# Kernel optimization log

Hardware: AMD Instinct MI355X
Metric: run time of the kernel (lower is better)

Reference implementation:

```python
import jax, jax.numpy as jnp
import numpy as np

B, T, DZ = 128, 512, 512  # batch, timesteps, latent state dim


def setup_inputs() -> dict:
    key = jax.random.key(0)
    k1, k2, k3 = jax.random.split(key, 3)
    t_inputs = jax.random.normal(k1, (B, T, 1), dtype=jnp.float32)      # per-step scalar time signal
    init_states = jax.random.normal(k2, (B, DZ), dtype=jnp.float32)     # initial latent state z_0
    f = jax.random.normal(k3, (1, DZ), dtype=jnp.float32) * 0.05        # learned weight f (D_in=1, D_z)
    return {"t_inputs": t_inputs, "init_states": init_states, "f": f}


def reference(t_inputs, init_states, f):
    # keras.backend.rnn with step: z_t = x_t * f + z_{t-1}
    # This linear recurrence is exactly a left-to-right prefix sum:
    #   z_t = z_0 + sum_{s<=t} x_s * f
    # outputs[1] of K.rnn is the full stacked sequence (B, T, DZ).
    increments = t_inputs * f                       # (B,T,1)*(1,DZ) -> (B,T,DZ)
    return init_states[:, None, :] + jnp.cumsum(increments, axis=1)
```

## Files before the change

kernel.cpp:

```cpp
#include <hip/hip_runtime.h>

#define BB 128
#define TT 512
#define DZ 512
#define RPB 128
#define NBLOCKS ((BB * TT) / RPB)

typedef float f4_t __attribute__((ext_vector_type(4)));

__global__ __launch_bounds__(256, 4) void lts_kernel(
    const float* __restrict__ t_in,
    const float* __restrict__ init,
    const float* __restrict__ f,
    float* __restrict__ out)
{
    __shared__ float s[TT];

    const int tid = threadIdx.x;
    const int g0  = blockIdx.x * RPB;
    const int b   = g0 >> 9;
    const int t0  = g0 & (TT - 1);

    if (tid < 64) {
        const float* xb = t_in + b * TT + tid * 8;
        const f4_t a = *reinterpret_cast<const f4_t*>(xb);
        const f4_t c = *reinterpret_cast<const f4_t*>(xb + 4);
        const float v0 = a.x;
        const float v1 = v0 + a.y;
        const float v2 = v1 + a.z;
        const float v3 = v2 + a.w;
        const float v4 = v3 + c.x;
        const float v5 = v4 + c.y;
        const float v6 = v5 + c.z;
        const float v7 = v6 + c.w;
        float run = v7;
#pragma unroll
        for (int off = 1; off < 64; off <<= 1) {
            const float y = __shfl_up(run, off, 64);
            if (tid >= off) run += y;
        }
        const float excl = run - v7;
        f4_t o0, o1;
        o0.x = v0 + excl; o0.y = v1 + excl; o0.z = v2 + excl; o0.w = v3 + excl;
        o1.x = v4 + excl; o1.y = v5 + excl; o1.z = v6 + excl; o1.w = v7 + excl;
        *reinterpret_cast<f4_t*>(&s[tid * 8])     = o0;
        *reinterpret_cast<f4_t*>(&s[tid * 8 + 4]) = o1;
    }

    const int q = tid & 127;
    const int h = tid >> 7;
    const int d = q * 4;

    const f4_t f4 = *reinterpret_cast<const f4_t*>(&f[d]);
    const f4_t i4 = *reinterpret_cast<const f4_t*>(&init[b * DZ + d]);

    __syncthreads();

    float* outp = out + ((size_t)(g0 + h) * DZ + d);
#pragma unroll 8
    for (int iter = 0; iter < RPB / 2; ++iter) {
        const float st = s[t0 + iter * 2 + h];
        f4_t o;
        o.x = i4.x + f4.x * st;
        o.y = i4.y + f4.y * st;
        o.z = i4.z + f4.z * st;
        o.w = i4.w + f4.w * st;
        __builtin_nontemporal_store(o, reinterpret_cast<f4_t*>(outp));
        outp += 2 * DZ;
    }
}

extern "C" void kernel_launch(void* const* d_in, const int* in_sizes, int n_in,
                              void* d_out, int out_size, void* d_ws, size_t ws_size,
                              hipStream_t stream) {
    const float* t_in = (const float*)d_in[0];
    const float* init = (const float*)d_in[1];
    const float* f    = (const float*)d_in[2];
    float* out        = (float*)d_out;

    lts_kernel<<<dim3(NBLOCKS), dim3(256), 0, stream>>>(t_in, init, f, out);
}
```

Measured before the change: 29.16 us.

## Give each wave its own redundant scan to drop block barrier

Every wave now computes the full 512-element prefix sum of its batch row into a private shared-memory slice. This removes the __syncthreads and the idle waves that previously waited on a single scanning wave. Each lane now writes 8 contiguous floats (two float4 stores) per row, and each wave handles every fourth row. Nontemporal stores are replaced with ordinary stores. The cost is 4x redundant input loads and scan work per block, plus 4x the shared memory.

```diff
diff --git a/kernel.cpp b/kernel.cpp
--- a/kernel.cpp
+++ b/kernel.cpp
@@ -14,59 +14,61 @@
     const float* __restrict__ f,
     float* __restrict__ out)
 {
-    __shared__ float s[TT];
+    __shared__ float s[4][TT];
 
-    const int tid = threadIdx.x;
-    const int g0  = blockIdx.x * RPB;
-    const int b   = g0 >> 9;
-    const int t0  = g0 & (TT - 1);
+    const int tid  = threadIdx.x;
+    const int wave = tid >> 6;
+    const int lane = tid & 63;
+    const int g0   = blockIdx.x * RPB;
+    const int b    = g0 >> 9;
+    const int t0   = g0 & (TT - 1);
 
-    if (tid < 64) {
-        const float* xb = t_in + b * TT + tid * 8;
-        const f4_t a = *reinterpret_cast<const f4_t*>(xb);
-        const f4_t c = *reinterpret_cast<const f4_t*>(xb + 4);
-        const float v0 = a.x;
-        const float v1 = v0 + a.y;
-        const float v2 = v1 + a.z;
-        const float v3 = v2 + a.w;
-        const float v4 = v3 + c.x;
-        const float v5 = v4 + c.y;
-        const float v6 = v5 + c.z;
-        const float v7 = v6 + c.w;
-        float run = v7;
+    const int d = lane * 8;
+    const f4_t fa = *reinterpret_cast<const f4_t*>(&f[d]);
+    const f4_t fb = *reinterpret_cast<const f4_t*>(&f[d + 4]);
+    const f4_t ia = *reinterpret_cast<const f4_t*>(&init[b * DZ + d]);
+    const f4_t ib = *reinterpret_cast<const f4_t*>(&init[b * DZ + d + 4]);
+
+    const float* xb = t_in + b * TT + lane * 8;
+    const f4_t a = *reinterpret_cast<const f4_t*>(xb);
+    const f4_t c = *reinterpret_cast<const f4_t*>(xb + 4);
+    const float v0 = a.x;
+    const float v1 = v0 + a.y;
+    const float v2 = v1 + a.z;
+    const float v3 = v2 + a.w;
+    const float v4 = v3 + c.x;
+    const float v5 = v4 + c.y;
+    const float v6 = v5 + c.z;
+    const float v7 = v6 + c.w;
+    float run = v7;
 #pragma unroll
-        for (int off = 1; off < 64; off <<= 1) {
-            const float y = __shfl_up(run, off, 64);
-            if (tid >= off) run += y;
-        }
-        const float excl = run - v7;
-        f4_t o0, o1;
-        o0.x = v0 + excl; o0.y = v1 + excl; o0.z = v2 + excl; o0.w = v3 + excl;
-        o1.x = v4 + excl; o1.y = v5 + excl; o1.z = v6 + excl; o1.w = v7 + excl;
-        *reinterpret_cast<f4_t*>(&s[tid * 8])     = o0;
-        *reinterpret_cast<f4_t*>(&s[tid * 8 + 4]) = o1;
+    for (int off = 1; off < 64; off <<= 1) {
+        const float y = __shfl_up(run, off, 64);
+        if (lane >= off) run += y;
     }
+    const float excl = run - v7;
+    f4_t o0, o1;
+    o0.x = v0 + excl; o0.y = v1 + excl; o0.z = v2 + excl; o0.w = v3 + excl;
+    o1.x = v4 + excl; o1.y = v5 + excl; o1.z = v6 + excl; o1.w = v7 + excl;
+    *reinterpret_cast<f4_t*>(&s[wave][lane * 8])     = o0;
+    *reinterpret_cast<f4_t*>(&s[wave][lane * 8 + 4]) = o1;
 
-    const int q = tid & 127;
-    const int h = tid >> 7;
-    const int d = q * 4;
-
-    const f4_t f4 = *reinterpret_cast<const f4_t*>(&f[d]);
-    const f4_t i4 = *reinterpret_cast<const f4_t*>(&init[b * DZ + d]);
-
-    __syncthreads();
-
-    float* outp = out + ((size_t)(g0 + h) * DZ + d);
+    float* outp = out + ((size_t)(g0 + wave) * DZ + d);
 #pragma unroll 8
-    for (int iter = 0; iter < RPB / 2; ++iter) {
-        const float st = s[t0 + iter * 2 + h];
-        f4_t o;
-        o.x = i4.x + f4.x * st;
-        o.y = i4.y + f4.y * st;
-        o.z = i4.z + f4.z * st;
-        o.w = i4.w + f4.w * st;
-        __builtin_nontemporal_store(o, reinterpret_cast<f4_t*>(outp));
-        outp += 2 * DZ;
+    for (int iter = 0; iter < RPB / 4; ++iter) {
+        const float st = s[wave][t0 + iter * 4 + wave];
+        f4_t oA, oB;
+        oA.x = ia.x + fa.x * st;
+        oA.y = ia.y + fa.y * st;
+        oA.z = ia.z + fa.z * st;
+        oA.w = ia.w + fa.w * st;
+        oB.x = ib.x + fb.x * st;
+        oB.y = ib.y + fb.y * st;
+        oB.z = ib.z + fb.z * st;
+        oB.w = ib.w + fb.w * st;
+        *reinterpret_cast<f4_t*>(outp)     = oA;
+        *reinterpret_cast<f4_t*>(outp + 4) = oB;
+        outp += 4 * DZ;
     }
 }
 
```

Result: no change. 28.81 us (-1.2%).
